# Kernel optimization log

Hardware: AMD Instinct MI355X
Metric: run time of the kernel (lower is better)

The kernel has to match this reference:

```python
import jax, jax.numpy as jnp
import numpy as np

B, T, D, H = 1, 4096, 1024, 16
DK = D // H
SCALE = 1.0 / float(np.sqrt(DK))
NEG = -1e9


def setup_inputs() -> dict:
    key = jax.random.key(0)
    k1, k2, k3 = jax.random.split(key, 3)
    x = jax.random.normal(k1, (B, T, D), dtype=jnp.float32)
    # xavier-ish small weights (gain 0.5)
    Wqkv = jax.random.normal(k2, (3 * D, D), dtype=jnp.float32) * 0.02
    Wout = jax.random.normal(k3, (D, D), dtype=jnp.float32) * 0.02
    return {"x": x, "Wqkv": Wqkv, "Wout": Wout}


def reference(x, Wqkv, Wout):
    b, t, d = x.shape
    # QKV projection (no bias): [B,T,3D] -> [3,B,H,T,DK]
    qkv = jnp.einsum('btd,ed->bte', x, Wqkv)
    qkv = qkv.reshape(b, t, 3, H, DK).transpose(2, 0, 3, 1, 4)
    q, k, v = qkv[0], qkv[1], qkv[2]
    # scaled dot-product scores, clamped
    scores = jnp.einsum('bhtd,bhsd->bhts', q, k) * SCALE
    scores = jnp.clip(scores, -10.0, 10.0)
    # causal additive mask (strict upper triangle gets -1e9)
    mask = jnp.triu(jnp.full((t, t), NEG, dtype=scores.dtype), k=1)
    scores = scores + mask[None, None, :, :]
    attn = jax.nn.softmax(scores, axis=-1)  # dropout is identity in eval
    out = jnp.einsum('bhts,bhsd->bhtd', attn, v)
    out = out.transpose(0, 2, 1, 3).reshape(b, t, d)
    return jnp.einsum('btd,ed->bte', out, Wout)
```

## Files before the change

kernel.cpp:

```cpp
#include <hip/hip_runtime.h>

#define T_SEQ   4096
#define D_MODEL 1024
#define NH      16
#define HD      64
#define E3      3072
#define QSCL    0.125f
#define TILEB   (64L*E3)
#define SLOTSZ  16896
#define P0CAP   800

using u32x2  = __attribute__((ext_vector_type(2))) unsigned int;
using u32x4  = __attribute__((ext_vector_type(4))) unsigned int;
using u16x4  = __attribute__((ext_vector_type(4))) unsigned short;
using u16x8  = __attribute__((ext_vector_type(8))) unsigned short;
using u64x2  = __attribute__((ext_vector_type(2))) unsigned long long;
using f32x4  = __attribute__((ext_vector_type(4))) float;
using bf16x8 = __attribute__((ext_vector_type(8))) __bf16;

__device__ __forceinline__ unsigned short f2bf(float f){
  unsigned int u = __builtin_bit_cast(unsigned int, f);
  u += 0x7fffu + ((u >> 16) & 1u);
  return (unsigned short)(u >> 16);
}
__device__ __forceinline__ float bf2f(unsigned short v){
  unsigned int u = ((unsigned int)v) << 16;
  return __builtin_bit_cast(float, u);
}

__device__ __forceinline__ void gload_lds16(const void* g, void* l){
  __builtin_amdgcn_global_load_lds((const __attribute__((address_space(1))) void*)g,
                                   (__attribute__((address_space(3))) void*)l, 16, 0, 0);
}

__device__ __forceinline__ char* part_ptr(char* p0, char* p1, int slot){
  return (slot < P0CAP) ? p0 + (size_t)slot * SLOTSZ
                        : p1 + (size_t)(slot - P0CAP) * SLOTSZ;
}

#define XN4   (T_SEQ*D_MODEL/4)
#define WQN4  (E3*D_MODEL/4)
#define WON4  (D_MODEL*D_MODEL/4)
__global__ __launch_bounds__(256) void cvt_all(const float4* __restrict__ x,
                                               const float4* __restrict__ wq,
                                               const float4* __restrict__ wo,
                                               u16x4* __restrict__ xb,
                                               u16x4* __restrict__ wqb,
                                               u16x4* __restrict__ wob){
  int i = blockIdx.x * 256 + threadIdx.x;
  const float4* src; u16x4* dst; int j;
  if(i < XN4){ src = x;  dst = xb;  j = i; }
  else if(i < XN4 + WQN4){ src = wq; dst = wqb; j = i - XN4; }
  else { src = wo; dst = wob; j = i - XN4 - WQN4; }
  float4 v = src[j];
  u16x4 o = { f2bf(v.x), f2bf(v.y), f2bf(v.z), f2bf(v.w) };
  dst[j] = o;
}

template<int OUT_BF16, int QSCALE>
__global__ __launch_bounds__(256) void gemm_bt(const unsigned short* __restrict__ A,
                                               const unsigned short* __restrict__ B,
                                               void* __restrict__ Cv,
                                               int M, int N, int K){
  __shared__ unsigned short As[128*64];
  __shared__ unsigned short Bs[128*64];
  const int t    = threadIdx.x;
  const int lane = t & 63;
  const int w    = t >> 6;
  const int cc   = lane & 15;
  const int gg   = lane >> 4;

  const int nbx  = N >> 7;
  const int cpx  = gridDim.x >> 3;
  const int wg   = (blockIdx.x & 7) * cpx + (blockIdx.x >> 3);
  const int brow = (wg / nbx) * 128;
  const int bcol = (wg % nbx) * 128;
  const int wrow = (w >> 1) * 64;
  const int wcol = (w & 1) * 64;

  f32x4 acc[4][4];
  #pragma unroll
  for(int m=0;m<4;++m)
    #pragma unroll
    for(int n=0;n<4;++n)
      acc[m][n] = (f32x4){0.f,0.f,0.f,0.f};

  const int  srow = t >> 3;
  const int  schk = ((t & 7) ^ (srow & 7)) * 8;
  const long aBase = (long)(brow + srow) * K + schk;
  const long bBase = (long)(bcol + srow) * K + schk;

  const int kOff0 = cc*128 + (((gg    ) ^ (cc&7)) << 4);
  const int kOff1 = cc*128 + (((gg + 4) ^ (cc&7)) << 4);

  for(int k0 = 0; k0 < K; k0 += 64){
    __syncthreads();
    #pragma unroll
    for(int p=0;p<4;++p){
      gload_lds16(A + aBase + k0 + (long)p*32*K, (char*)As + p*4096 + t*16);
      gload_lds16(B + bBase + k0 + (long)p*32*K, (char*)Bs + p*4096 + t*16);
    }
    __syncthreads();

    #pragma unroll
    for(int kk=0;kk<2;++kk){
      const int off = kk ? kOff1 : kOff0;
      bf16x8 af[4], bfr[4];
      #pragma unroll
      for(int m=0;m<4;++m)
        af[m]  = *(const bf16x8*)((const char*)As + wrow*128 + m*2048 + off);
      #pragma unroll
      for(int n=0;n<4;++n)
        bfr[n] = *(const bf16x8*)((const char*)Bs + wcol*128 + n*2048 + off);
      #pragma unroll
      for(int m=0;m<4;++m)
        #pragma unroll
        for(int n=0;n<4;++n)
          acc[m][n] = __builtin_amdgcn_mfma_f32_16x16x32_bf16(af[m], bfr[n], acc[m][n], 0, 0, 0);
    }
  }

  #pragma unroll
  for(int m=0;m<4;++m){
    #pragma unroll
    for(int n=0;n<4;++n){
      const int row0 = brow + wrow + m*16 + gg*4;
      const int col  = bcol + wcol + n*16 + cc;
      const float sc = (QSCALE && col < D_MODEL) ? QSCL : 1.0f;
      #pragma unroll
      for(int r=0;r<4;++r){
        if constexpr (OUT_BF16 != 0){
          ((unsigned short*)Cv)[(long)(row0 + r)*N + col] = f2bf(acc[m][n][r] * sc);
        } else {
          ((float*)Cv)[(long)(row0 + r)*N + col] = acc[m][n][r];
        }
      }
    }
  }
}

__global__ __launch_bounds__(256) void gemm_bt64(const unsigned short* __restrict__ A,
                                                 const unsigned short* __restrict__ B,
                                                 float* __restrict__ C,
                                                 int M, int N, int K){
  __shared__ unsigned short As[64*32];
  __shared__ unsigned short Bs[128*32];
  const int t    = threadIdx.x;
  const int lane = t & 63;
  const int w    = t >> 6;
  const int brow = blockIdx.y * 64;
  const int bcol = blockIdx.x * 128;
  const int wrow = (w >> 1) * 32;
  const int wcol = (w & 1) * 64;
  const int cc = lane & 15;
  const int gg = lane >> 4;

  f32x4 acc[2][4];
  #pragma unroll
  for(int m=0;m<2;++m)
    #pragma unroll
    for(int n=0;n<4;++n)
      acc[m][n] = (f32x4){0.f,0.f,0.f,0.f};

  const int srow = t >> 2;
  const int sk   = (t & 3) * 8;
  const long aBase = (long)(brow + srow) * K;
  const long bBase = (long)(bcol + srow) * K;

  for(int k0 = 0; k0 < K; k0 += 32){
    __syncthreads();
    gload_lds16(A + aBase + k0 + sk,               As + t*8);
    gload_lds16(B + bBase + k0 + sk,               Bs + t*8);
    gload_lds16(B + bBase + 64*(long)K + k0 + sk,  Bs + 2048 + t*8);
    __syncthreads();

    bf16x8 af[2], bfr[4];
    #pragma unroll
    for(int m=0;m<2;++m)
      af[m]  = *(const bf16x8*)((const char*)As + (wrow + m*16 + cc)*64 + gg*16);
    #pragma unroll
    for(int n=0;n<4;++n)
      bfr[n] = *(const bf16x8*)((const char*)Bs + (wcol + n*16 + cc)*64 + gg*16);
    #pragma unroll
    for(int m=0;m<2;++m)
      #pragma unroll
      for(int n=0;n<4;++n)
        acc[m][n] = __builtin_amdgcn_mfma_f32_16x16x32_bf16(af[m], bfr[n], acc[m][n], 0, 0, 0);
  }

  #pragma unroll
  for(int m=0;m<2;++m){
    #pragma unroll
    for(int n=0;n<4;++n){
      const int row0 = brow + wrow + m*16 + gg*4;
      const int col  = bcol + wcol + n*16 + cc;
      #pragma unroll
      for(int r=0;r<4;++r)
        C[(long)(row0 + r)*N + col] = acc[m][n][r];
    }
  }
}

__global__ __launch_bounds__(256, 3) void attn_part(const unsigned short* __restrict__ qkv,
                                                    unsigned short* __restrict__ attnb,
                                                    char* __restrict__ parts0,
                                                    char* __restrict__ parts1){
  __shared__ char LB[32768];

  const int t    = threadIdx.x;
  const int lane = t & 63;
  const int w    = t >> 6;
  const int cc   = lane & 15;
  const int gg   = lane >> 4;

  const int bid  = blockIdx.x;
  const int hd   = bid & 15;
  const int o_   = bid >> 4;
  const int item = (o_ < 8) ? (7 - o_) : (95 - o_);

  int QB, t0, n, slot;
  if(item < 8){
    QB = item; t0 = 0; n = 2*QB + 2; slot = -1;
  } else if(item < 24){
    const int i = item - 8; QB = 8 + (i >> 1); const int hf = i & 1;
    const int h0 = QB + 1;
    t0 = hf * h0; n = h0;
    slot = (hd*8 + (QB-8))*2 + hf;
  } else {
    const int i = item - 24; QB = 16 + (i >> 2); const int qt = i & 3;
    const int n0 = 2*QB + 2, bsz = n0 >> 2, rem = n0 & 3;
    t0 = qt*bsz + (qt < rem ? qt : rem);
    n  = bsz + (qt < rem ? 1 : 0);
    slot = 256 + (hd*16 + (QB-16))*4 + qt;
  }
  const int gA = 2*QB;
  const int qA = QB*128 + w*16;

  bf16x8 bqA0 = *(const bf16x8*)(qkv + (long)(qA+cc)*E3 + hd*HD +      gg*8);
  bf16x8 bqA1 = *(const bf16x8*)(qkv + (long)(qA+cc)*E3 + hd*HD + 32 + gg*8);
  bf16x8 bqB0 = *(const bf16x8*)(qkv + (long)(qA+64+cc)*E3 + hd*HD +      gg*8);
  bf16x8 bqB1 = *(const bf16x8*)(qkv + (long)(qA+64+cc)*E3 + hd*HD + 32 + gg*8);

  const f32x4 z4 = (f32x4){0.f,0.f,0.f,0.f};
  f32x4 accA0=z4, accA1=z4, accA2=z4, accA3=z4;
  f32x4 accB0=z4, accB1=z4, accB2=z4, accB3=z4;
  float rsA = 0.f, rsB = 0.f;

  const bool lb0 = (4*gg + 0) > cc;
  const bool lb1 = (4*gg + 1) > cc;
  const bool lb2 = (4*gg + 2) > cc;
  const bool lb3 = (4*gg + 3) > cc;

  const int kOffA = cc*128 + (((gg    ) ^ (cc&7)) << 4);
  const int kOffB = cc*128 + (((gg + 4) ^ (cc&7)) << 4);

  const unsigned ldsBase = (unsigned)(unsigned long long)(&LB[0]);
  const unsigned vA0 = ldsBase + 8192  + lane*8;
  const unsigned vA1 = ldsBase + 24576 + lane*8;

  const int kLane0 = (t>>3)*E3 + D_MODEL + hd*HD + (((t&7) ^ ((t>>3)&7)) << 3);
  const int kLane1 = kLane0 + 32*E3;
  const int vLane0 = (4*((t>>3)&15) + ((t&7)>>1))*E3 + 2*D_MODEL + hd*HD
                     + ((2*(t>>7) + (t&1)) << 3);
  const int vLane1 = vLane0 + 32;

  #define STAGE(g_, BUF) do{                                                       \
    const unsigned short* gb_ = qkv + (long)(g_)*TILEB;                            \
    gload_lds16(gb_ + kLane0, LB + (BUF)*16384 + t*16);                            \
    gload_lds16(gb_ + kLane1, LB + (BUF)*16384 + 4096  + t*16);                    \
    gload_lds16(gb_ + vLane0, LB + (BUF)*16384 + 8192  + t*16);                    \
    gload_lds16(gb_ + vLane1, LB + (BUF)*16384 + 12288 + t*16);                    \
  }while(0)

  #define TRRD(d_, va_, OFF_)                                                      \
    asm volatile("ds_read_b64_tr_b16 %0, %1 offset:%c2"                            \
                 : "=v"(d_) : "v"(va_), "i"(OFF_))

  #define PVHALF(vab_, HOFF, doA_, doB_)                                           \
  {                                                                                \
    unsigned long long q0_,q1_,q2_,q3_,q4_,q5_,q6_,q7_;                            \
    TRRD(q0_, vab_, (HOFF) + 0);    TRRD(q1_, vab_, (HOFF) + 512);                 \
    TRRD(q2_, vab_, (HOFF) + 2048); TRRD(q3_, vab_, (HOFF) + 2560);                \
    TRRD(q4_, vab_, (HOFF) + 4096); TRRD(q5_, vab_, (HOFF) + 4608);                \
    TRRD(q6_, vab_, (HOFF) + 6144); TRRD(q7_, vab_, (HOFF) + 6656);                \
    asm volatile("s_waitcnt lgkmcnt(0)");                                          \
    __builtin_amdgcn_sched_barrier(0);                                             \
    u64x2 w0_ = {q0_,q1_}; bf16x8 bv0_ = __builtin_bit_cast(bf16x8, w0_);          \
    u64x2 w1_ = {q2_,q3_}; bf16x8 bv1_ = __builtin_bit_cast(bf16x8, w1_);          \
    u64x2 w2_ = {q4_,q5_}; bf16x8 bv2_ = __builtin_bit_cast(bf16x8, w2_);          \
    u64x2 w3_ = {q6_,q7_}; bf16x8 bv3_ = __builtin_bit_cast(bf16x8, w3_);          \
    if(doA_){                                                                      \
      accA0 = __builtin_amdgcn_mfma_f32_16x16x32_bf16(paA_, bv0_, accA0, 0,0,0);   \
      accA1 = __builtin_amdgcn_mfma_f32_16x16x32_bf16(paA_, bv1_, accA1, 0,0,0);   \
      accA2 = __builtin_amdgcn_mfma_f32_16x16x32_bf16(paA_, bv2_, accA2, 0,0,0);   \
      accA3 = __builtin_amdgcn_mfma_f32_16x16x32_bf16(paA_, bv3_, accA3, 0,0,0);   \
    }                                                                              \
    if(doB_){                                                                      \
      accB0 = __builtin_amdgcn_mfma_f32_16x16x32_bf16(paB_, bv0_, accB0, 0,0,0);   \
      accB1 = __builtin_amdgcn_mfma_f32_16x16x32_bf16(paB_, bv1_, accB1, 0,0,0);   \
      accB2 = __builtin_amdgcn_mfma_f32_16x16x32_bf16(paB_, bv2_, accB2, 0,0,0);   \
      accB3 = __builtin_amdgcn_mfma_f32_16x16x32_bf16(paB_, bv3_, accB3, 0,0,0);   \
    }                                                                              \
  }

  #define PACK4(pk_) (bf16x8){ (__bf16)pk_[0][0],(__bf16)pk_[0][1],(__bf16)pk_[0][2],\
    (__bf16)pk_[0][3],(__bf16)pk_[1][0],(__bf16)pk_[1][1],(__bf16)pk_[1][2],        \
    (__bf16)pk_[1][3] }
  #define PACK4H(pk_) (bf16x8){ (__bf16)pk_[2][0],(__bf16)pk_[2][1],(__bf16)pk_[2][2],\
    (__bf16)pk_[2][3],(__bf16)pk_[3][0],(__bf16)pk_[3][1],(__bf16)pk_[3][2],        \
    (__bf16)pk_[3][3] }

  #define TILE_INT(g_, BUF)                                                        \
  {                                                                                \
    STAGE((g_)+1, (BUF)^1);                                                        \
    const char* kb_ = (const char*)LB + (BUF)*16384;                               \
    float pkA[4][4], pkB[4][4];                                                    \
    _Pragma("unroll")                                                              \
    for(int kt=0; kt<4; ++kt){                                                     \
      bf16x8 a0 = *(const bf16x8*)(kb_ + kOffA + kt*2048);                         \
      bf16x8 a1 = *(const bf16x8*)(kb_ + kOffB + kt*2048);                         \
      f32x4 sA = __builtin_amdgcn_mfma_f32_16x16x32_bf16(a0, bqA0, z4, 0,0,0);     \
      sA = __builtin_amdgcn_mfma_f32_16x16x32_bf16(a1, bqA1, sA, 0,0,0);           \
      f32x4 sB = __builtin_amdgcn_mfma_f32_16x16x32_bf16(a0, bqB0, z4, 0,0,0);     \
      sB = __builtin_amdgcn_mfma_f32_16x16x32_bf16(a1, bqB1, sB, 0,0,0);           \
      _Pragma("unroll")                                                            \
      for(int rr=0; rr<4; ++rr){                                                   \
        float pA_ = __expf(__builtin_amdgcn_fmed3f(sA[rr], -10.f, 10.f));          \
        float pB_ = __expf(__builtin_amdgcn_fmed3f(sB[rr], -10.f, 10.f));          \
        rsA += pA_; rsB += pB_;                                                    \
        pkA[kt][rr] = pA_; pkB[kt][rr] = pB_;                                      \
      }                                                                            \
    }                                                                              \
    bf16x8 paA_, paB_;                                                             \
    const unsigned vab_ = (BUF) ? vA1 : vA0;                                       \
    paA_ = PACK4(pkA);  paB_ = PACK4(pkB);                                         \
    PVHALF(vab_, 0, 1, 1);                                                         \
    paA_ = PACK4H(pkA); paB_ = PACK4H(pkB);                                        \
    PVHALF(vab_, 1024, 1, 1);                                                      \
    __syncthreads();                                                               \
  }

  #define TILE_TAIL(g_, BUFR)                                                      \
  {                                                                                \
    STAGE((g_)+1, (BUFR)^1);                                                       \
    const char* kb_ = (const char*)LB + (BUFR)*16384;                              \
    float pkA[4][4], pkB[4][4];                                                    \
    const bool dA_ = ((g_) == gA);                                                 \
    _Pragma("unroll")                                                              \
    for(int kt=0; kt<4; ++kt){                                                     \
      bf16x8 a0 = *(const bf16x8*)(kb_ + kOffA + kt*2048);                         \
      bf16x8 a1 = *(const bf16x8*)(kb_ + kOffB + kt*2048);                         \
      if(dA_){                                                                     \
        f32x4 sB = __builtin_amdgcn_mfma_f32_16x16x32_bf16(a0, bqB0, z4, 0,0,0);   \
        sB = __builtin_amdgcn_mfma_f32_16x16x32_bf16(a1, bqB1, sB, 0,0,0);         \
        _Pragma("unroll")                                                          \
        for(int rr=0; rr<4; ++rr){                                                 \
          float pB_ = __expf(__builtin_amdgcn_fmed3f(sB[rr], -10.f, 10.f));        \
          rsB += pB_; pkB[kt][rr] = pB_;                                           \
        }                                                                          \
        if(kt <= w){                                                               \
          f32x4 sA = __builtin_amdgcn_mfma_f32_16x16x32_bf16(a0, bqA0, z4, 0,0,0); \
          sA = __builtin_amdgcn_mfma_f32_16x16x32_bf16(a1, bqA1, sA, 0,0,0);       \
          float p0_ = __expf(__builtin_amdgcn_fmed3f(sA[0], -10.f, 10.f));         \
          float p1_ = __expf(__builtin_amdgcn_fmed3f(sA[1], -10.f, 10.f));         \
          float p2_ = __expf(__builtin_amdgcn_fmed3f(sA[2], -10.f, 10.f));         \
          float p3_ = __expf(__builtin_amdgcn_fmed3f(sA[3], -10.f, 10.f));         \
          if(kt == w){                                                             \
            p0_ = lb0 ? 0.f : p0_;  p1_ = lb1 ? 0.f : p1_;                         \
            p2_ = lb2 ? 0.f : p2_;  p3_ = lb3 ? 0.f : p3_;                         \
          }                                                                        \
          rsA += p0_ + p1_ + p2_ + p3_;                                            \
          pkA[kt][0]=p0_; pkA[kt][1]=p1_; pkA[kt][2]=p2_; pkA[kt][3]=p3_;          \
        } else {                                                                   \
          pkA[kt][0]=0.f; pkA[kt][1]=0.f; pkA[kt][2]=0.f; pkA[kt][3]=0.f;          \
        }                                                                          \
      } else {                                                                     \
        pkA[kt][0]=0.f; pkA[kt][1]=0.f; pkA[kt][2]=0.f; pkA[kt][3]=0.f;            \
        if(kt <= w){                                                               \
          f32x4 sB = __builtin_amdgcn_mfma_f32_16x16x32_bf16(a0, bqB0, z4, 0,0,0); \
          sB = __builtin_amdgcn_mfma_f32_16x16x32_bf16(a1, bqB1, sB, 0,0,0);       \
          float p0_ = __expf(__builtin_amdgcn_fmed3f(sB[0], -10.f, 10.f));         \
          float p1_ = __expf(__builtin_amdgcn_fmed3f(sB[1], -10.f, 10.f));         \
          float p2_ = __expf(__builtin_amdgcn_fmed3f(sB[2], -10.f, 10.f));         \
          float p3_ = __expf(__builtin_amdgcn_fmed3f(sB[3], -10.f, 10.f));         \
          if(kt == w){                                                             \
            p0_ = lb0 ? 0.f : p0_;  p1_ = lb1 ? 0.f : p1_;                         \
            p2_ = lb2 ? 0.f : p2_;  p3_ = lb3 ? 0.f : p3_;                         \
          }                                                                        \
          rsB += p0_ + p1_ + p2_ + p3_;                                            \
          pkB[kt][0]=p0_; pkB[kt][1]=p1_; pkB[kt][2]=p2_; pkB[kt][3]=p3_;          \
        } else {                                                                   \
          pkB[kt][0]=0.f; pkB[kt][1]=0.f; pkB[kt][2]=0.f; pkB[kt][3]=0.f;          \
        }                                                                          \
      }                                                                            \
    }                                                                              \
    bf16x8 paA_, paB_;                                                             \
    const unsigned vab_ = (BUFR) ? vA1 : vA0;                                      \
    paA_ = PACK4(pkA);  paB_ = PACK4(pkB);                                         \
    PVHALF(vab_, 0, dA_, 1);                                                       \
    paA_ = PACK4H(pkA); paB_ = PACK4H(pkB);                                        \
    if(w >= 2){ PVHALF(vab_, 1024, dA_, 1); }                                      \
    else if(dA_){ PVHALF(vab_, 1024, 0, 1); }                                      \
    __syncthreads();                                                               \
  }

  STAGE(t0, 0);
  __syncthreads();

  const int gap  = gA - t0;
  const int nInt = (n < gap) ? n : (gap < 0 ? 0 : gap);
  int lt = 0;
  while(lt + 2 <= nInt){
    TILE_INT(t0+lt,   0);
    TILE_INT(t0+lt+1, 1);
    lt += 2;
  }
  if(lt < nInt){ TILE_INT(t0+lt, 0); ++lt; }
  if(lt < n){ TILE_TAIL(t0+lt, (lt&1)); ++lt; }
  if(lt < n){ TILE_TAIL(t0+lt, (lt&1)); ++lt; }

  rsA += __shfl_xor(rsA, 16);  rsA += __shfl_xor(rsA, 32);
  rsB += __shfl_xor(rsB, 16);  rsB += __shfl_xor(rsB, 32);

  if(slot < 0){
    #pragma unroll
    for(int rr=0;rr<4;++rr){
      const float invA = 1.0f / __shfl(rsA, 4*gg + rr);
      const int rowA = qA + 4*gg + rr;
      unsigned short* dA = attnb + (long)rowA*D_MODEL + hd*HD + cc;
      dA[0]  = __builtin_bit_cast(unsigned short, (__bf16)(accA0[rr]*invA));
      dA[16] = __builtin_bit_cast(unsigned short, (__bf16)(accA1[rr]*invA));
      dA[32] = __builtin_bit_cast(unsigned short, (__bf16)(accA2[rr]*invA));
      dA[48] = __builtin_bit_cast(unsigned short, (__bf16)(accA3[rr]*invA));
      const float invB = 1.0f / __shfl(rsB, 4*gg + rr);
      unsigned short* dB = dA + 64L*D_MODEL;
      dB[0]  = __builtin_bit_cast(unsigned short, (__bf16)(accB0[rr]*invB));
      dB[16] = __builtin_bit_cast(unsigned short, (__bf16)(accB1[rr]*invB));
      dB[32] = __builtin_bit_cast(unsigned short, (__bf16)(accB2[rr]*invB));
      dB[48] = __builtin_bit_cast(unsigned short, (__bf16)(accB3[rr]*invB));
    }
  } else {
    char* sp = part_ptr(parts0, parts1, slot);
    #pragma unroll
    for(int rr=0;rr<4;++rr){
      const int rowA = w*16 + 4*gg + rr;
      unsigned short* dA = (unsigned short*)sp + rowA*64 + cc;
      dA[0]  = f2bf(accA0[rr]);
      dA[16] = f2bf(accA1[rr]);
      dA[32] = f2bf(accA2[rr]);
      dA[48] = f2bf(accA3[rr]);
      unsigned short* dB = dA + 64*64;
      dB[0]  = f2bf(accB0[rr]);
      dB[16] = f2bf(accB1[rr]);
      dB[32] = f2bf(accB2[rr]);
      dB[48] = f2bf(accB3[rr]);
    }
    if(gg == 0){
      ((float*)(sp + 16384))[w*16 + cc]      = rsA;
      ((float*)(sp + 16384))[64 + w*16 + cc] = rsB;
    }
  }
  #undef STAGE
  #undef TRRD
  #undef PVHALF
  #undef PACK4
  #undef PACK4H
  #undef TILE_INT
  #undef TILE_TAIL
}

__global__ __launch_bounds__(256) void attn_combine(char* __restrict__ parts0,
                                                    char* __restrict__ parts1,
                                                    unsigned short* __restrict__ attnb){
  const int b  = blockIdx.x;
  const int hd = b & 15;
  const int QB = 8 + (b >> 4);
  const int t  = threadIdx.x;
  const int r  = t >> 1;
  const int d0 = (t & 1) * 32;

  int s0_, np;
  if(QB < 16){ s0_ = (hd*8 + (QB-8))*2;        np = 2; }
  else       { s0_ = 256 + (hd*16 + (QB-16))*4; np = 4; }

  float rs = 0.f;
  float o[32];
  #pragma unroll
  for(int j=0;j<32;++j) o[j] = 0.f;

  for(int pi = 0; pi < np; ++pi){
    const char* pp = part_ptr(parts0, parts1, s0_ + pi);
    rs += ((const float*)(pp + 16384))[r];
    #pragma unroll
    for(int q=0;q<4;++q){
      u16x8 a = *(const u16x8*)(pp + (r*64 + d0 + q*8)*2);
      #pragma unroll
      for(int j=0;j<8;++j) o[q*8+j] += bf2f(a[j]);
    }
  }
  const float inv = 1.0f / rs;
  unsigned short* dst = attnb + (long)(QB*128 + r)*D_MODEL + hd*HD + d0;
  #pragma unroll
  for(int q=0;q<4;++q){
    u16x8 ov;
    #pragma unroll
    for(int j=0;j<8;++j) ov[j] = f2bf(o[q*8+j]*inv);
    *(u16x8*)(dst + q*8) = ov;
  }
}

extern "C" void kernel_launch(void* const* d_in, const int* in_sizes, int n_in,
                              void* d_out, int out_size, void* d_ws, size_t ws_size,
                              hipStream_t stream){
  (void)in_sizes; (void)n_in; (void)out_size; (void)ws_size;
  const float* x    = (const float*)d_in[0];
  const float* wqkv = (const float*)d_in[1];
  const float* wout = (const float*)d_in[2];
  char* ws = (char*)d_ws;
  unsigned short* woutb = (unsigned short*)(ws);
  unsigned short* attnb = (unsigned short*)(ws + (2u  << 20));
  unsigned short* qkvb  = (unsigned short*)(ws + (10u << 20));
  unsigned short* xb    = (unsigned short*)(ws + (34u << 20));
  unsigned short* wqkvb = (unsigned short*)(ws + (42u << 20));
  char*           parts0 = ws + (34u << 20);
  char*           parts1 = (char*)d_out;
  float* out = (float*)d_out;

  cvt_all<<<dim3((XN4 + WQN4 + WON4)/256), 256, 0, stream>>>(
      (const float4*)x, (const float4*)wqkv, (const float4*)wout,
      (u16x4*)xb, (u16x4*)wqkvb, (u16x4*)woutb);

  gemm_bt<1,1><<<dim3((T_SEQ/128)*(E3/128)), 256, 0, stream>>>(xb, wqkvb, qkvb, T_SEQ, E3, D_MODEL);

  attn_part<<<dim3(88*NH), 256, 0, stream>>>(qkvb, attnb, parts0, parts1);
  attn_combine<<<dim3(24*NH), 256, 0, stream>>>(parts0, parts1, attnb);

  dim3 g3(D_MODEL/128, T_SEQ/64);
  gemm_bt64<<<g3, 256, 0, stream>>>(attnb, woutb, out, T_SEQ, D_MODEL, D_MODEL);
}
```

Before: 117.7 us.

## Split long causal query blocks 8-way and deepen output-projection GEMM K-tile

The attention partition is reworked so the last query blocks (QB 24-31) are split into 8 key-range parts instead of 4, and the issue order is changed so split items run first. The grid grows from 88 to 120 items per head. The output-projection GEMM switches to a K-tile of 64 with XOR-swizzled LDS layout to avoid bank conflicts, and to a 1D grid remapped across 8 XCD groups. The aims are better load balance for the longest causal rows and fewer loop iterations and syncs in the GEMM. The cost is more partial buffers and combine work, and the combine grid may not cover the new slot layout. The parts buffer also grows, which risks overlapping other workspace regions.

```diff
diff --git a/kernel.cpp b/kernel.cpp
--- a/kernel.cpp
+++ b/kernel.cpp
@@ -143,17 +143,21 @@
                                                  const unsigned short* __restrict__ B,
                                                  float* __restrict__ C,
                                                  int M, int N, int K){
-  __shared__ unsigned short As[64*32];
-  __shared__ unsigned short Bs[128*32];
+  __shared__ unsigned short As[64*64];
+  __shared__ unsigned short Bs[128*64];
   const int t    = threadIdx.x;
   const int lane = t & 63;
   const int w    = t >> 6;
-  const int brow = blockIdx.y * 64;
-  const int bcol = blockIdx.x * 128;
+  const int cc   = lane & 15;
+  const int gg   = lane >> 4;
+
+  const int nbx  = N >> 7;
+  const int cpx  = gridDim.x >> 3;
+  const int wg   = (blockIdx.x & 7) * cpx + (blockIdx.x >> 3);
+  const int brow = (wg / nbx) * 64;
+  const int bcol = (wg % nbx) * 128;
   const int wrow = (w >> 1) * 32;
   const int wcol = (w & 1) * 64;
-  const int cc = lane & 15;
-  const int gg = lane >> 4;
 
   f32x4 acc[2][4];
   #pragma unroll
@@ -162,30 +166,40 @@
     for(int n=0;n<4;++n)
       acc[m][n] = (f32x4){0.f,0.f,0.f,0.f};
 
-  const int srow = t >> 2;
-  const int sk   = (t & 3) * 8;
-  const long aBase = (long)(brow + srow) * K;
-  const long bBase = (long)(bcol + srow) * K;
-
-  for(int k0 = 0; k0 < K; k0 += 32){
+  const int  srow = t >> 3;
+  const int  schk = ((t & 7) ^ (srow & 7)) * 8;
+  const long aBase = (long)(brow + srow) * K + schk;
+  const long bBase = (long)(bcol + srow) * K + schk;
+
+  const int kOff0 = cc*128 + (((gg    ) ^ (cc&7)) << 4);
+  const int kOff1 = cc*128 + (((gg + 4) ^ (cc&7)) << 4);
+
+  for(int k0 = 0; k0 < K; k0 += 64){
     __syncthreads();
-    gload_lds16(A + aBase + k0 + sk,               As + t*8);
-    gload_lds16(B + bBase + k0 + sk,               Bs + t*8);
-    gload_lds16(B + bBase + 64*(long)K + k0 + sk,  Bs + 2048 + t*8);
+    #pragma unroll
+    for(int p=0;p<2;++p)
+      gload_lds16(A + aBase + k0 + (long)p*32*K, (char*)As + p*4096 + t*16);
+    #pragma unroll
+    for(int p=0;p<4;++p)
+      gload_lds16(B + bBase + k0 + (long)p*32*K, (char*)Bs + p*4096 + t*16);
     __syncthreads();
 
-    bf16x8 af[2], bfr[4];
-    #pragma unroll
-    for(int m=0;m<2;++m)
-      af[m]  = *(const bf16x8*)((const char*)As + (wrow + m*16 + cc)*64 + gg*16);
-    #pragma unroll
-    for(int n=0;n<4;++n)
-      bfr[n] = *(const bf16x8*)((const char*)Bs + (wcol + n*16 + cc)*64 + gg*16);
-    #pragma unroll
-    for(int m=0;m<2;++m)
+    #pragma unroll
+    for(int kk=0;kk<2;++kk){
+      const int off = kk ? kOff1 : kOff0;
+      bf16x8 af[2], bfr[4];
+      #pragma unroll
+      for(int m=0;m<2;++m)
+        af[m]  = *(const bf16x8*)((const char*)As + wrow*128 + m*2048 + off);
       #pragma unroll
       for(int n=0;n<4;++n)
-        acc[m][n] = __builtin_amdgcn_mfma_f32_16x16x32_bf16(af[m], bfr[n], acc[m][n], 0, 0, 0);
+        bfr[n] = *(const bf16x8*)((const char*)Bs + wcol*128 + n*2048 + off);
+      #pragma unroll
+      for(int m=0;m<2;++m)
+        #pragma unroll
+        for(int n=0;n<4;++n)
+          acc[m][n] = __builtin_amdgcn_mfma_f32_16x16x32_bf16(af[m], bfr[n], acc[m][n], 0, 0, 0);
+    }
   }
 
   #pragma unroll
@@ -216,22 +230,27 @@
   const int bid  = blockIdx.x;
   const int hd   = bid & 15;
   const int o_   = bid >> 4;
-  const int item = (o_ < 8) ? (7 - o_) : (95 - o_);
 
   int QB, t0, n, slot;
-  if(item < 8){
-    QB = item; t0 = 0; n = 2*QB + 2; slot = -1;
-  } else if(item < 24){
-    const int i = item - 8; QB = 8 + (i >> 1); const int hf = i & 1;
+  if(o_ < 16){
+    QB = 15 - (o_ >> 1); const int hf = o_ & 1;
     const int h0 = QB + 1;
     t0 = hf * h0; n = h0;
     slot = (hd*8 + (QB-8))*2 + hf;
-  } else {
-    const int i = item - 24; QB = 16 + (i >> 2); const int qt = i & 3;
+  } else if(o_ < 24){
+    QB = 23 - o_; t0 = 0; n = 2*QB + 2; slot = -1;
+  } else if(o_ < 56){
+    const int i = o_ - 24; QB = 23 - (i >> 2); const int qt = i & 3;
     const int n0 = 2*QB + 2, bsz = n0 >> 2, rem = n0 & 3;
     t0 = qt*bsz + (qt < rem ? qt : rem);
     n  = bsz + (qt < rem ? 1 : 0);
-    slot = 256 + (hd*16 + (QB-16))*4 + qt;
+    slot = 256 + (hd*8 + (QB-16))*4 + qt;
+  } else {
+    const int i = o_ - 56; QB = 31 - (i >> 3); const int qt = i & 7;
+    const int n0 = 2*QB + 2, bsz = n0 >> 3, rem = n0 & 7;
+    t0 = qt*bsz + (qt < rem ? qt : rem);
+    n  = bsz + (qt < rem ? 1 : 0);
+    slot = 768 + (hd*8 + (QB-24))*8 + qt;
   }
   const int gA = 2*QB;
   const int qA = QB*128 + w*16;
@@ -480,8 +499,9 @@
   const int d0 = (t & 1) * 32;
 
   int s0_, np;
-  if(QB < 16){ s0_ = (hd*8 + (QB-8))*2;        np = 2; }
-  else       { s0_ = 256 + (hd*16 + (QB-16))*4; np = 4; }
+  if(QB < 16)      { s0_ = (hd*8 + (QB-8))*2;         np = 2; }
+  else if(QB < 24) { s0_ = 256 + (hd*8 + (QB-16))*4;  np = 4; }
+  else             { s0_ = 768 + (hd*8 + (QB-24))*8;  np = 8; }
 
   float rs = 0.f;
   float o[32];
@@ -532,9 +552,8 @@
 
   gemm_bt<1,1><<<dim3((T_SEQ/128)*(E3/128)), 256, 0, stream>>>(xb, wqkvb, qkvb, T_SEQ, E3, D_MODEL);
 
-  attn_part<<<dim3(88*NH), 256, 0, stream>>>(qkvb, attnb, parts0, parts1);
+  attn_part<<<dim3(120*NH), 256, 0, stream>>>(qkvb, attnb, parts0, parts1);
   attn_combine<<<dim3(24*NH), 256, 0, stream>>>(parts0, parts1, attnb);
 
-  dim3 g3(D_MODEL/128, T_SEQ/64);
-  gemm_bt64<<<g3, 256, 0, stream>>>(attnb, woutb, out, T_SEQ, D_MODEL, D_MODEL);
-}
+  gemm_bt64<<<dim3((T_SEQ/64)*(D_MODEL/128)), 256, 0, stream>>>(attnb, woutb, out, T_SEQ, D_MODEL, D_MODEL);
+}
```

Result: faster. 114.6 us (median of 3 runs) (-2.6%).
